# Kernel tuning notes

Measured on AMD Instinct MI355X. Metric: run time of the kernel, lower is better.

## Reference

```python
import jax, jax.numpy as jnp
import numpy as np

B, S, HID, NH, HD = 2, 2048, 1024, 16, 64
SCALE = 1.0 / np.sqrt(HD)
NEG = -1e9


def _rope_cache(seq_len, dim, base=10000.0):
    inv_freq = 1.0 / (base ** (np.arange(0, dim, 2, dtype=np.float32) / dim))
    t = np.arange(seq_len, dtype=np.float32)
    freqs = np.outer(t, inv_freq)                      # [S, dim/2]
    emb = np.concatenate([freqs, freqs], axis=-1)      # [S, dim]
    return jnp.asarray(np.cos(emb)), jnp.asarray(np.sin(emb))


def _rotate_half(x):
    x1, x2 = jnp.split(x, 2, axis=-1)
    return jnp.concatenate([-x2, x1], axis=-1)


def setup_inputs() -> dict:
    key = jax.random.key(0)
    k0, k1, k2, k3, k4 = jax.random.split(key, 5)
    hidden_states = jax.random.normal(k0, (B, S, HID), jnp.float32)
    Wq = jax.random.normal(k1, (HID, NH * HD), jnp.float32) * 0.02
    Wk = jax.random.normal(k2, (HID, NH * HD), jnp.float32) * 0.02
    Wv = jax.random.normal(k3, (HID, NH * HD), jnp.float32) * 0.02
    Wo = jax.random.normal(k4, (NH * HD, HID), jnp.float32) * 0.02
    causal = jnp.tril(jnp.ones((S, S), bool))
    attention_mask = jnp.broadcast_to(
        jnp.where(causal, 0.0, NEG).astype(jnp.float32)[None, None], (B, 1, S, S))
    position_ids = jnp.broadcast_to(jnp.arange(S, dtype=jnp.int32)[None], (B, S))
    cos, sin = _rope_cache(S, HD)
    return {"hidden_states": hidden_states, "attention_mask": attention_mask,
            "position_ids": position_ids, "cos": cos, "sin": sin,
            "Wq": Wq, "Wk": Wk, "Wv": Wv, "Wo": Wo}


def reference(hidden_states, attention_mask, position_ids, cos, sin, Wq, Wk, Wv, Wo):
    b, s, _ = hidden_states.shape
    def proj(W):  # [B,S,HID] @ [HID,NH*HD] -> [B,NH,S,HD]
        return jnp.einsum('bsh,hd->bsd', hidden_states, W).reshape(b, s, NH, HD).transpose(0, 2, 1, 3)
    q, k, v = proj(Wq), proj(Wk), proj(Wv)
    # RoPE: gather per-position cos/sin -> [B,1,S,HD]
    cos_g = cos[position_ids][:, None]
    sin_g = sin[position_ids][:, None]
    q = q * cos_g + _rotate_half(q) * sin_g
    k = k * cos_g + _rotate_half(k) * sin_g
    scores = jnp.einsum('bhqd,bhkd->bhqk', q, k) * SCALE + attention_mask
    attn = jax.nn.softmax(scores.astype(jnp.float32), axis=-1).astype(q.dtype)
    out = jnp.einsum('bhqk,bhkd->bhqd', attn, v)
    out = out.transpose(0, 2, 1, 3).reshape(b, s, NH * HD)
    return jnp.einsum('bsd,dh->bsh', out, Wo)
```

## Files before the change

kernel.cpp:

```cpp
#include <hip/hip_runtime.h>

typedef __bf16 bf16x8 __attribute__((ext_vector_type(8)));
typedef float  f32x4  __attribute__((ext_vector_type(4)));
typedef unsigned short ushortx8 __attribute__((ext_vector_type(8)));
typedef unsigned short ushortx4 __attribute__((ext_vector_type(4)));

static __device__ __forceinline__ unsigned short f2bf(float f) {
  unsigned int u = __builtin_bit_cast(unsigned int, f);
  u += 0x7FFFu + ((u >> 16) & 1u);
  return (unsigned short)(u >> 16);
}
static __device__ __forceinline__ unsigned short f2bf_fast(float f) {
  unsigned int u = __builtin_bit_cast(unsigned int, f);
  return (unsigned short)((u + 0x8000u) >> 16);
}

#define GLL16(gp, lp) __builtin_amdgcn_global_load_lds(                       \
    (const __attribute__((address_space(1))) void*)(gp),                      \
    (__attribute__((address_space(3))) void*)(lp), 16, 0, 0)

__global__ __launch_bounds__(256) void prep_kernel(const float* __restrict__ X,
                                                   const float* __restrict__ W0,
                                                   const float* __restrict__ W1,
                                                   const float* __restrict__ W2,
                                                   const float* __restrict__ W3,
                                                   unsigned short* __restrict__ Xbf,
                                                   unsigned short* __restrict__ D0,
                                                   unsigned short* __restrict__ D1,
                                                   unsigned short* __restrict__ D2,
                                                   unsigned short* __restrict__ D3) {
  int z = blockIdx.z;
  if (z >= 4) {
    long bid = (long)(z - 4) * 1024 + blockIdx.y * 32 + blockIdx.x;
    int tl = threadIdx.y * 32 + threadIdx.x;
    long i = bid * 2048 + (long)tl * 8;
    float4 f0 = *(const float4*)(X + i);
    float4 f1 = *(const float4*)(X + i + 4);
    ushortx8 u;
    u[0] = f2bf(f0.x); u[1] = f2bf(f0.y); u[2] = f2bf(f0.z); u[3] = f2bf(f0.w);
    u[4] = f2bf(f1.x); u[5] = f2bf(f1.y); u[6] = f2bf(f1.z); u[7] = f2bf(f1.w);
    *(ushortx8*)(Xbf + i) = u;
    return;
  }
  const float* src = (z == 0) ? W0 : (z == 1) ? W1 : (z == 2) ? W2 : W3;
  unsigned short* dst = (z == 0) ? D0 : (z == 1) ? D1 : (z == 2) ? D2 : D3;
  const int R = 1024, C = 1024;
  __shared__ unsigned short t[32][33];
  int c = blockIdx.x * 32 + threadIdx.x;
#pragma unroll
  for (int i = 0; i < 4; ++i) {
    int r = blockIdx.y * 32 + threadIdx.y + i * 8;
    t[threadIdx.y + i * 8][threadIdx.x] = f2bf(src[(size_t)r * C + c]);
  }
  __syncthreads();
  int rr = blockIdx.y * 32 + threadIdx.x;
#pragma unroll
  for (int i = 0; i < 4; ++i) {
    int cc = blockIdx.x * 32 + threadIdx.y + i * 8;
    dst[(size_t)cc * R + rr] = t[threadIdx.x][threadIdx.y + i * 8];
  }
}

__global__ __launch_bounds__(256, 3) void qkvr_kernel(
    const unsigned short* __restrict__ A,
    const unsigned short* __restrict__ BT0,
    const unsigned short* __restrict__ BT1,
    const unsigned short* __restrict__ BT2,
    unsigned short* __restrict__ outQ,
    unsigned short* __restrict__ outK,
    unsigned short* __restrict__ outVT,
    const int* __restrict__ pos_ids,
    const float* __restrict__ cosb,
    const float* __restrict__ sinb) {
  const int K = 1024;
  int id = blockIdx.x + 8 * (blockIdx.y + 32 * blockIdx.z);
  int m_idx = id & 31;
  int nzi = id >> 5;
  int n_idx = nzi & 7;
  int z = nzi >> 3;
  const unsigned short* BT = (z == 0) ? BT0 : (z == 1 ? BT1 : BT2);
  int n0 = n_idx * 128, m0 = m_idx * 128;
  int t = threadIdx.x, lane = t & 63, w = t >> 6;
  int wy = w >> 1, wx = w & 1;
  int n16 = lane & 15, quad = lane >> 4;

  __shared__ __align__(16) unsigned short sA[3][128][32];
  __shared__ __align__(16) unsigned short sB[3][128][32];
  __shared__ __align__(16) unsigned short sDummy[512];
  const int BUFE = 128 * 32;

  int r4 = lane >> 2, c4 = lane & 3;
  const char* gA = (const char*)(A + (size_t)(m0 + w * 32 + r4) * K) + ((c4 ^ (r4 & 3)) * 16);
  const char* gB = (const char*)(BT + (size_t)(n0 + w * 32 + r4) * K) + ((c4 ^ (r4 & 3)) * 16);
  const size_t row16 = (size_t)16 * K * 2;
  unsigned short* stA = &sA[0][w * 32][0];
  unsigned short* stB = &sB[0][w * 32][0];

  int cs = (quad ^ (n16 & 3)) * 8;
  const unsigned short* rdA = &sA[0][wy * 64 + n16][0] + cs;
  const unsigned short* rdB = &sB[0][wx * 64 + n16][0] + cs;

  f32x4 acc[4][4];
#pragma unroll
  for (int i = 0; i < 4; ++i)
#pragma unroll
    for (int j = 0; j < 4; ++j) acc[i][j] = f32x4{0.f, 0.f, 0.f, 0.f};

  bf16x8 a[4], b[4];

#define QSTG(tt, dA, dB)                                                        \
  do {                                                                          \
    GLL16(gA + (size_t)(tt) * 64, (dA));                                        \
    GLL16(gA + (size_t)(tt) * 64 + row16, (dA) + 16 * 32);                      \
    GLL16(gB + (size_t)(tt) * 64, (dB));                                        \
    GLL16(gB + (size_t)(tt) * 64 + row16, (dB) + 16 * 32);                      \
  } while (0)

#define QRD(bufi)                                                               \
  do {                                                                          \
    _Pragma("unroll") for (int i = 0; i < 4; ++i) {                             \
      a[i] = *(const bf16x8*)(rdA + (bufi) * BUFE + (i * 16) * 32);             \
      b[i] = *(const bf16x8*)(rdB + (bufi) * BUFE + (i * 16) * 32);             \
    }                                                                           \
  } while (0)

#define QMM                                                                     \
  do {                                                                          \
    _Pragma("unroll") for (int mt = 0; mt < 4; ++mt)                            \
      _Pragma("unroll") for (int nt = 0; nt < 4; ++nt)                          \
        acc[mt][nt] = __builtin_amdgcn_mfma_f32_16x16x32_bf16(                  \
            a[mt], b[nt], acc[mt][nt], 0, 0, 0);                                \
  } while (0)

  QSTG(0, stA, stB);
  QSTG(1, stA + BUFE, stB + BUFE);
  asm volatile("s_waitcnt vmcnt(4)" ::: "memory");
  __builtin_amdgcn_s_barrier();

#pragma unroll 3
  for (int kt = 0; kt < 30; ++kt) {
    int buf = kt % 3;
    int pfb = (kt + 2) % 3;
    QRD(buf);
    QSTG(kt + 2, stA + pfb * BUFE, stB + pfb * BUFE);
    QMM;
    asm volatile("s_waitcnt vmcnt(4)" ::: "memory");
    __builtin_amdgcn_s_barrier();
  }
  {
    QRD(0);
    QSTG(31, sDummy, sDummy);
    QMM;
    asm volatile("s_waitcnt vmcnt(4)" ::: "memory");
    __builtin_amdgcn_s_barrier();
  }
  {
    QRD(1);
    QSTG(31, sDummy, sDummy);
    QMM;
    asm volatile("s_waitcnt vmcnt(0)" ::: "memory");
  }
#undef QSTG
#undef QRD
#undef QMM

  if (z < 2) {
    const float qs = (z == 0) ? (0.125f * 1.44269504088896340736f) : 1.0f;
#pragma unroll
    for (int mt = 0; mt < 4; ++mt)
#pragma unroll
      for (int r = 0; r < 4; ++r) {
        int row = m0 + wy * 64 + mt * 16 + quad * 4 + r;
        int b_ = row >> 11, s_ = row & 2047;
        int pos = pos_ids[b_ * 2048 + s_];
        const float* cb = cosb + (size_t)pos * 64;
        const float* sb = sinb + (size_t)pos * 64;
#pragma unroll
        for (int nt = 0; nt < 2; ++nt) {
          int d0 = nt * 16 + n16;
          float c0 = cb[d0] * qs, s0 = sb[d0] * qs;
          float c1 = cb[d0 + 32] * qs, s1 = sb[d0 + 32] * qs;
          float x0 = acc[mt][nt][r], x1 = acc[mt][nt + 2][r];
          acc[mt][nt][r]     = x0 * c0 - x1 * s0;
          acc[mt][nt + 2][r] = x1 * c1 + x0 * s1;
        }
      }
    unsigned short* dst = (z == 0) ? outQ : outK;
#pragma unroll
    for (int mt = 0; mt < 4; ++mt)
#pragma unroll
      for (int nt = 0; nt < 4; ++nt)
#pragma unroll
        for (int r = 0; r < 4; ++r) {
          int row = m0 + wy * 64 + mt * 16 + quad * 4 + r;
          int col = n0 + wx * 64 + nt * 16 + n16;
          int b_ = row >> 11, s_ = row & 2047, h_ = col >> 6, d_ = col & 63;
          dst[(((size_t)b_ * 16 + h_) * 2048 + s_) * 64 + d_] = f2bf(acc[mt][nt][r]);
        }
    return;
  }

#pragma unroll
  for (int mt = 0; mt < 4; ++mt)
#pragma unroll
    for (int nt = 0; nt < 4; ++nt) {
      int row = m0 + wy * 64 + mt * 16 + quad * 4;
      int b_ = row >> 11, s_ = row & 2047;
      int col = n0 + wx * 64 + nt * 16 + n16;
      int h_ = col >> 6, d_ = col & 63;
      ushortx4 u;
#pragma unroll
      for (int r = 0; r < 4; ++r) u[r] = f2bf(acc[mt][nt][r]);
      *(ushortx4*)(&outVT[(((size_t)b_ * 16 + h_) * 64 + d_) * 2048 + s_]) = u;
    }
}

__global__ __launch_bounds__(256) void wor_kernel(const unsigned short* __restrict__ A,
                                                  const unsigned short* __restrict__ BT,
                                                  float* __restrict__ outF) {
  const int K = 1024, N = 1024;
  int id = blockIdx.x + 8 * blockIdx.y;
  int m_idx = id & 31, n_idx = id >> 5;
  int m0 = m_idx * 128, n0 = n_idx * 64;
  int t = threadIdx.x, lane = t & 63, w = t >> 6;
  int wy = w >> 1, wx = w & 1;
  int n16 = lane & 15, quad = lane >> 4;

  __shared__ __align__(16) unsigned short sA[3][128][32];
  __shared__ __align__(16) unsigned short sB[3][64][32];
  __shared__ __align__(16) unsigned short sDummy[512];
  const int BUFA = 128 * 32, BUFB = 64 * 32;

  int r4 = lane >> 2, c4 = lane & 3;
  const char* gA = (const char*)(A + (size_t)(m0 + w * 32 + r4) * K) + ((c4 ^ (r4 & 3)) * 16);
  const char* gB = (const char*)(BT + (size_t)(n0 + w * 16 + r4) * K) + ((c4 ^ (r4 & 3)) * 16);
  const size_t row16 = (size_t)16 * K * 2;
  unsigned short* stA = &sA[0][w * 32][0];
  unsigned short* stB = &sB[0][w * 16][0];

  int cs = (quad ^ (n16 & 3)) * 8;
  const unsigned short* rdA = &sA[0][wy * 64 + n16][0] + cs;
  const unsigned short* rdB = &sB[0][wx * 32 + n16][0] + cs;

  f32x4 acc[4][2];
#pragma unroll
  for (int i = 0; i < 4; ++i)
#pragma unroll
    for (int j = 0; j < 2; ++j) acc[i][j] = f32x4{0.f, 0.f, 0.f, 0.f};

  bf16x8 a[4], b[2];

#define WSTG(tt, dA, dB)                                                        \
  do {                                                                          \
    GLL16(gA + (size_t)(tt) * 64, (dA));                                        \
    GLL16(gA + (size_t)(tt) * 64 + row16, (dA) + 16 * 32);                      \
    GLL16(gB + (size_t)(tt) * 64, (dB));                                        \
  } while (0)

#define WRD(bufi)                                                               \
  do {                                                                          \
    _Pragma("unroll") for (int i = 0; i < 4; ++i)                               \
      a[i] = *(const bf16x8*)(rdA + (bufi) * BUFA + (i * 16) * 32);             \
    _Pragma("unroll") for (int j = 0; j < 2; ++j)                               \
      b[j] = *(const bf16x8*)(rdB + (bufi) * BUFB + (j * 16) * 32);             \
  } while (0)

#define WMM                                                                     \
  do {                                                                          \
    _Pragma("unroll") for (int mt = 0; mt < 4; ++mt)                            \
      _Pragma("unroll") for (int nt = 0; nt < 2; ++nt)                          \
        acc[mt][nt] = __builtin_amdgcn_mfma_f32_16x16x32_bf16(                  \
            a[mt], b[nt], acc[mt][nt], 0, 0, 0);                                \
  } while (0)

  WSTG(0, stA, stB);
  WSTG(1, stA + BUFA, stB + BUFB);
  asm volatile("s_waitcnt vmcnt(3)" ::: "memory");
  __builtin_amdgcn_s_barrier();

#pragma unroll 3
  for (int kt = 0; kt < 30; ++kt) {
    int buf = kt % 3;
    int pfb = (kt + 2) % 3;
    WRD(buf);
    WSTG(kt + 2, stA + pfb * BUFA, stB + pfb * BUFB);
    WMM;
    asm volatile("s_waitcnt vmcnt(3)" ::: "memory");
    __builtin_amdgcn_s_barrier();
  }
  {
    WRD(0);
    WSTG(31, sDummy, sDummy);
    WMM;
    asm volatile("s_waitcnt vmcnt(3)" ::: "memory");
    __builtin_amdgcn_s_barrier();
  }
  {
    WRD(1);
    WSTG(31, sDummy, sDummy);
    WMM;
    asm volatile("s_waitcnt vmcnt(0)" ::: "memory");
  }
#undef WSTG
#undef WRD
#undef WMM

#pragma unroll
  for (int mt = 0; mt < 4; ++mt)
#pragma unroll
    for (int nt = 0; nt < 2; ++nt)
#pragma unroll
      for (int r = 0; r < 4; ++r) {
        int row = m0 + wy * 64 + mt * 16 + quad * 4 + r;
        int col = n0 + wx * 32 + nt * 16 + n16;
        outF[(size_t)row * N + col] = acc[mt][nt][r];
      }
}

__global__ __launch_bounds__(512) void attn_kernel(const unsigned short* __restrict__ Q,
                                                   const unsigned short* __restrict__ Kk,
                                                   const unsigned short* __restrict__ VT,
                                                   unsigned short* __restrict__ O) {
  int bh = blockIdx.x;
  int qt = (int)(gridDim.y - 1 - blockIdx.y);
  int t = threadIdx.x;
  int lane = t & 63;
  int w = t >> 6;
  int g = w >> 2;
  int w4 = w & 3;
  int n16 = lane & 15, quad = lane >> 4;
  int r8 = lane >> 3, c8 = lane & 7;
  const unsigned short* Qb = Q + (size_t)bh * 2048 * 64;
  const unsigned short* Kb = Kk + (size_t)bh * 2048 * 64;
  const unsigned short* Vb = VT + (size_t)bh * 64 * 2048;

  __shared__ __align__(16) unsigned short sKV[2 * 2 * 2 * 4096];
  __shared__ __align__(16) unsigned short sP[8][16 * 64];
  unsigned short* spW = sP[w];
  unsigned short* gBase = sKV + g * 16384;

  int b_ = bh >> 4, h_ = bh & 15;
  int nk = qt + 1;
  int u = (nk + 1) >> 1;
  int beg = g ? u : 0;
  int end = g ? nk : u;
  int qg = qt * 64 + w4 * 16 + n16;

  bf16x8 aQ[2];
#pragma unroll
  for (int kb = 0; kb < 2; ++kb)
    aQ[kb] = *(const bf16x8*)(Qb + (size_t)qg * 64 + kb * 32 + quad * 8);

  f32x4 o[4];
  float mst = -3e38f, lst = 0.f;
#pragma unroll
  for (int ct = 0; ct < 4; ++ct) o[ct] = f32x4{0.f, 0.f, 0.f, 0.f};

#define ASTAGE(kt_, BUF)                                                                  \
  do {                                                                                    \
    const unsigned short* kg_ = Kb + (size_t)((kt_) * 64 + w4 * 16) * 64;                 \
    const unsigned short* vg_ = Vb + (size_t)(w4 * 16) * 2048 + (kt_) * 64;               \
    unsigned short* dK = gBase + (BUF) * 8192 + (w4 * 16) * 64;                           \
    unsigned short* dV = dK + 4096;                                                       \
    GLL16(kg_ + (size_t)r8 * 64 + (c8 ^ r8) * 8, dK);                                     \
    GLL16(kg_ + (size_t)(8 + r8) * 64 + (c8 ^ r8) * 8, dK + 8 * 64);                      \
    GLL16(vg_ + (size_t)r8 * 2048 + (c8 ^ r8) * 8, dV);                                   \
    GLL16(vg_ + (size_t)(8 + r8) * 2048 + (c8 ^ r8) * 8, dV + 8 * 64);                    \
  } while (0)

#define ACOMPUTE(kt_, BUF)                                                                \
  do {                                                                                    \
    const unsigned short* kT_ = gBase + (BUF) * 8192;                                     \
    const unsigned short* vT_ = kT_ + 4096;                                               \
    f32x4 sc[4];                                \
    _Pragma("unroll") for (int mt = 0; mt < 4; ++mt) {                                    \
      const unsigned short* kr = &kT_[(mt * 16 + n16) * 64];                              \
      bf16x8 ka0 = *(const bf16x8*)(kr + ((quad ^ (n16 & 7)) * 8));                       \
      bf16x8 ka1 = *(const bf16x8*)(kr + (((4 + quad) ^ (n16 & 7)) * 8));                 \
      f32x4 zv = f32x4{0.f, 0.f, 0.f, 0.f};                                               \
      zv = __builtin_amdgcn_mfma_f32_16x16x32_bf16(ka0, aQ[0], zv, 0, 0, 0);              \
      sc[mt] = __builtin_amdgcn_mfma_f32_16x16x32_bf16(ka1, aQ[1], zv, 0, 0, 0);          \
    }                                                                                     \
    float p[4][4];                                                                        \
    _Pragma("unroll") for (int mt = 0; mt < 4; ++mt)                                      \
      _Pragma("unroll") for (int r = 0; r < 4; ++r) p[mt][r] = sc[mt][r];                 \
    if ((kt_) == nk - 1) {                                 \
      int kb0 = (kt_) * 64 + quad * 4;                                                    \
      _Pragma("unroll") for (int mt = 0; mt < 4; ++mt)                                    \
        _Pragma("unroll") for (int r = 0; r < 4; ++r)                                     \
          if (kb0 + mt * 16 + r > qg) p[mt][r] = -3e38f;                                  \
    }                                                                                     \
    float rm = p[0][0];                                                                   \
    _Pragma("unroll") for (int mt = 0; mt < 4; ++mt)                                      \
      _Pragma("unroll") for (int r = 0; r < 4; ++r) rm = fmaxf(rm, p[mt][r]);             \
    rm = fmaxf(rm, __shfl_xor(rm, 16));                                                   \
    rm = fmaxf(rm, __shfl_xor(rm, 32));                                                   \
    if (!__all(rm <= mst + 8.f)) {        \
      float mn = fmaxf(mst, rm);                                                          \
      float al = exp2f(mst - mn);                                                         \
      mst = mn;                                                                           \
      lst *= al;                                                                          \
      _Pragma("unroll") for (int ct = 0; ct < 4; ++ct)                                    \
        _Pragma("unroll") for (int r = 0; r < 4; ++r) o[ct][r] *= al;                     \
    }                                                                                     \
    float rs = 0.f;                                                                       \
    _Pragma("unroll") for (int mt = 0; mt < 4; ++mt)                                      \
      _Pragma("unroll") for (int r = 0; r < 4; ++r) {                                     \
        p[mt][r] = exp2f(p[mt][r] - mst);                                                 \
        rs += p[mt][r];                                                                   \
      }                                                                                   \
    lst += rs;                                                                            \
    _Pragma("unroll") for (int mt = 0; mt < 4; ++mt) {                                    \
      ushortx4 uu;                                                                        \
      _Pragma("unroll") for (int r = 0; r < 4; ++r) uu[r] = f2bf_fast(p[mt][r]);          \
      int ch = (mt * 2 + (quad >> 1)) ^ (n16 & 7);                                        \
      *(ushortx4*)(&spW[n16 * 64 + ch * 8 + (quad & 1) * 4]) = uu;                        \
    }                                                                                     \
    __builtin_amdgcn_s_waitcnt(0xC07F);     \
    bf16x8 aP0 = *(const bf16x8*)(&spW[n16 * 64 + ((quad ^ (n16 & 7)) * 8)]);             \
    bf16x8 aP1 = *(const bf16x8*)(&spW[n16 * 64 + (((4 + quad) ^ (n16 & 7)) * 8)]);       \
    _Pragma("unroll") for (int ct = 0; ct < 4; ++ct) {                                    \
      const unsigned short* vr = &vT_[(ct * 16 + n16) * 64];                              \
      bf16x8 va0 = *(const bf16x8*)(vr + ((quad ^ (n16 & 7)) * 8));                       \
      bf16x8 va1 = *(const bf16x8*)(vr + (((4 + quad) ^ (n16 & 7)) * 8));                 \
      o[ct] = __builtin_amdgcn_mfma_f32_16x16x32_bf16(va0, aP0, o[ct], 0, 0, 0);          \
      o[ct] = __builtin_amdgcn_mfma_f32_16x16x32_bf16(va1, aP1, o[ct], 0, 0, 0);          \
    }                                                                                     \
  } while (0)

  if (beg < end) ASTAGE(beg, 0);
  int it = 0;
  while (it < u) {
    __syncthreads();
    {
      int kt = beg + it;
      if (kt + 1 < end) ASTAGE(kt + 1, 1);
      if (kt < end) ACOMPUTE(kt, 0);
    }
    if (++it >= u) break;
    __syncthreads();
    {
      int kt = beg + it;
      if (kt + 1 < end) ASTAGE(kt + 1, 0);
      if (kt < end) ACOMPUTE(kt, 1);
    }
    ++it;
  }
#undef ASTAGE
#undef ACOMPUTE

  lst += __shfl_xor(lst, 16);
  lst += __shfl_xor(lst, 32);

  __syncthreads();
  float* scratch = (float*)sKV;
  int sidx = (w4 * 64 + lane) * 18;
  if (g == 1) {
#pragma unroll
    for (int ct = 0; ct < 4; ++ct)
#pragma unroll
      for (int r = 0; r < 4; ++r) scratch[sidx + ct * 4 + r] = o[ct][r];
    scratch[sidx + 16] = mst;
    scratch[sidx + 17] = lst;
  }
  __syncthreads();
  if (g == 0) {
    float m1 = scratch[sidx + 16], l1 = scratch[sidx + 17];
    float m = fmaxf(mst, m1);
    float a0 = exp2f(mst - m), a1 = exp2f(m1 - m);
    float inv = 1.0f / (lst * a0 + l1 * a1);
#pragma unroll
    for (int ct = 0; ct < 4; ++ct) {
      ushortx4 uo;
#pragma unroll
      for (int r = 0; r < 4; ++r) {
        float v = (o[ct][r] * a0 + scratch[sidx + ct * 4 + r] * a1) * inv;
        uo[r] = f2bf(v);
      }
      size_t addr = ((size_t)b_ * 2048 + qg) * 1024 + h_ * 64 + ct * 16 + quad * 4;
      *(ushortx4*)(&O[addr]) = uo;
    }
  }
}

extern "C" void kernel_launch(void* const* d_in, const int* in_sizes, int n_in,
                              void* d_out, int out_size, void* d_ws, size_t ws_size,
                              hipStream_t stream) {
  const float* X    = (const float*)d_in[0];
  const int*   pos  = (const int*)d_in[2];
  const float* cosb = (const float*)d_in[3];
  const float* sinb = (const float*)d_in[4];
  const float* Wq   = (const float*)d_in[5];
  const float* Wk   = (const float*)d_in[6];
  const float* Wv   = (const float*)d_in[7];
  const float* Wo   = (const float*)d_in[8];
  float* out = (float*)d_out;

  char* ws = (char*)d_ws;
  const size_t SZ_X = 4096UL * 1024 * 2;
  const size_t SZ_W = 1024UL * 1024 * 2;
  unsigned short* Xbf = (unsigned short*)(ws);
  unsigned short* WTq = (unsigned short*)(ws + SZ_X);
  unsigned short* WTk = (unsigned short*)(ws + SZ_X + SZ_W);
  unsigned short* WTv = (unsigned short*)(ws + SZ_X + 2 * SZ_W);
  unsigned short* WTo = (unsigned short*)(ws + SZ_X + 3 * SZ_W);
  unsigned short* Qbf = (unsigned short*)(ws + SZ_X + 4 * SZ_W);
  unsigned short* Kbf = (unsigned short*)(ws + 2 * SZ_X + 4 * SZ_W);
  unsigned short* VTr = (unsigned short*)(ws + 3 * SZ_X + 4 * SZ_W);
  unsigned short* Obf = (unsigned short*)(ws + 4 * SZ_X + 4 * SZ_W);

  prep_kernel<<<dim3(32, 32, 6), dim3(32, 8), 0, stream>>>(
      X, Wq, Wk, Wv, Wo, Xbf, WTq, WTk, WTv, WTo);

  qkvr_kernel<<<dim3(8, 32, 3), 256, 0, stream>>>(Xbf, WTq, WTk, WTv,
                                                  Qbf, Kbf, VTr,
                                                  pos, cosb, sinb);

  attn_kernel<<<dim3(32, 32), 512, 0, stream>>>(Qbf, Kbf, VTr, Obf);

  wor_kernel<<<dim3(8, 64), 256, 0, stream>>>(Obf, WTo, out);
}
```

Baseline: 201.7 us.

## Drop split-KV across two warp groups in causal attention kernel

The attention kernel previously split each query tile's key range between two groups of four waves and merged their partial softmax states through shared memory. The change removes the split, so one group of four waves walks the whole causal key range with double buffering, and the cross-group merge is gone. This halves threads and shared memory per block, allowing more resident blocks and removing the merge and two barriers. The cost is a longer serial loop per block, which may lengthen the critical path for the long diagonal tiles.

```diff
diff --git a/kernel.cpp b/kernel.cpp
--- a/kernel.cpp
+++ b/kernel.cpp
@@ -317,7 +317,7 @@
       }
 }
 
-__global__ __launch_bounds__(512) void attn_kernel(const unsigned short* __restrict__ Q,
+__global__ __launch_bounds__(256) void attn_kernel(const unsigned short* __restrict__ Q,
                                                    const unsigned short* __restrict__ Kk,
                                                    const unsigned short* __restrict__ VT,
                                                    unsigned short* __restrict__ O) {
@@ -326,25 +326,19 @@
   int t = threadIdx.x;
   int lane = t & 63;
   int w = t >> 6;
-  int g = w >> 2;
-  int w4 = w & 3;
   int n16 = lane & 15, quad = lane >> 4;
   int r8 = lane >> 3, c8 = lane & 7;
   const unsigned short* Qb = Q + (size_t)bh * 2048 * 64;
   const unsigned short* Kb = Kk + (size_t)bh * 2048 * 64;
   const unsigned short* Vb = VT + (size_t)bh * 64 * 2048;
 
-  __shared__ __align__(16) unsigned short sKV[2 * 2 * 2 * 4096];
-  __shared__ __align__(16) unsigned short sP[8][16 * 64];
+  __shared__ __align__(16) unsigned short sKV[2 * 8192];
+  __shared__ __align__(16) unsigned short sP[4][16 * 64];
   unsigned short* spW = sP[w];
-  unsigned short* gBase = sKV + g * 16384;
 
   int b_ = bh >> 4, h_ = bh & 15;
   int nk = qt + 1;
-  int u = (nk + 1) >> 1;
-  int beg = g ? u : 0;
-  int end = g ? nk : u;
-  int qg = qt * 64 + w4 * 16 + n16;
+  int qg = qt * 64 + w * 16 + n16;
 
   bf16x8 aQ[2];
 #pragma unroll
@@ -358,9 +352,9 @@
 
 #define ASTAGE(kt_, BUF)                                                                  \
   do {                                                                                    \
-    const unsigned short* kg_ = Kb + (size_t)((kt_) * 64 + w4 * 16) * 64;                 \
-    const unsigned short* vg_ = Vb + (size_t)(w4 * 16) * 2048 + (kt_) * 64;               \
-    unsigned short* dK = gBase + (BUF) * 8192 + (w4 * 16) * 64;                           \
+    const unsigned short* kg_ = Kb + (size_t)((kt_) * 64 + w * 16) * 64;                  \
+    const unsigned short* vg_ = Vb + (size_t)(w * 16) * 2048 + (kt_) * 64;                \
+    unsigned short* dK = sKV + (BUF) * 8192 + (w * 16) * 64;                              \
     unsigned short* dV = dK + 4096;                                                       \
     GLL16(kg_ + (size_t)r8 * 64 + (c8 ^ r8) * 8, dK);                                     \
     GLL16(kg_ + (size_t)(8 + r8) * 64 + (c8 ^ r8) * 8, dK + 8 * 64);                      \
@@ -370,7 +364,7 @@
 
 #define ACOMPUTE(kt_, BUF)                                                                \
   do {                                                                                    \
-    const unsigned short* kT_ = gBase + (BUF) * 8192;                                     \
+    const unsigned short* kT_ = sKV + (BUF) * 8192;                                       \
     const unsigned short* vT_ = kT_ + 4096;                                               \
     f32x4 sc[4];                                \
     _Pragma("unroll") for (int mt = 0; mt < 4; ++mt) {                                    \
@@ -428,21 +422,21 @@
     }                                                                                     \
   } while (0)
 
-  if (beg < end) ASTAGE(beg, 0);
+  ASTAGE(0, 0);
   int it = 0;
-  while (it < u) {
+  while (it < nk) {
     __syncthreads();
     {
-      int kt = beg + it;
-      if (kt + 1 < end) ASTAGE(kt + 1, 1);
-      if (kt < end) ACOMPUTE(kt, 0);
+      int kt = it;
+      if (kt + 1 < nk) ASTAGE(kt + 1, 1);
+      ACOMPUTE(kt, 0);
     }
-    if (++it >= u) break;
+    if (++it >= nk) break;
     __syncthreads();
     {
-      int kt = beg + it;
-      if (kt + 1 < end) ASTAGE(kt + 1, 0);
-      if (kt < end) ACOMPUTE(kt, 1);
+      int kt = it;
+      if (kt + 1 < nk) ASTAGE(kt + 1, 0);
+      ACOMPUTE(kt, 1);
     }
     ++it;
   }
@@ -451,35 +445,14 @@
 
   lst += __shfl_xor(lst, 16);
   lst += __shfl_xor(lst, 32);
-
-  __syncthreads();
-  float* scratch = (float*)sKV;
-  int sidx = (w4 * 64 + lane) * 18;
-  if (g == 1) {
-#pragma unroll
-    for (int ct = 0; ct < 4; ++ct)
-#pragma unroll
-      for (int r = 0; r < 4; ++r) scratch[sidx + ct * 4 + r] = o[ct][r];
-    scratch[sidx + 16] = mst;
-    scratch[sidx + 17] = lst;
-  }
-  __syncthreads();
-  if (g == 0) {
-    float m1 = scratch[sidx + 16], l1 = scratch[sidx + 17];
-    float m = fmaxf(mst, m1);
-    float a0 = exp2f(mst - m), a1 = exp2f(m1 - m);
-    float inv = 1.0f / (lst * a0 + l1 * a1);
-#pragma unroll
-    for (int ct = 0; ct < 4; ++ct) {
-      ushortx4 uo;
-#pragma unroll
-      for (int r = 0; r < 4; ++r) {
-        float v = (o[ct][r] * a0 + scratch[sidx + ct * 4 + r] * a1) * inv;
-        uo[r] = f2bf(v);
-      }
-      size_t addr = ((size_t)b_ * 2048 + qg) * 1024 + h_ * 64 + ct * 16 + quad * 4;
-      *(ushortx4*)(&O[addr]) = uo;
-    }
+  float inv = 1.0f / lst;
+#pragma unroll
+  for (int ct = 0; ct < 4; ++ct) {
+    ushortx4 uo;
+#pragma unroll
+    for (int r = 0; r < 4; ++r) uo[r] = f2bf(o[ct][r] * inv);
+    size_t addr = ((size_t)b_ * 2048 + qg) * 1024 + h_ * 64 + ct * 16 + quad * 4;
+    *(ushortx4*)(&O[addr]) = uo;
   }
 }
 
@@ -516,7 +489,7 @@
                                                   Qbf, Kbf, VTr,
                                                   pos, cosb, sinb);
 
-  attn_kernel<<<dim3(32, 32), 512, 0, stream>>>(Qbf, Kbf, VTr, Obf);
+  attn_kernel<<<dim3(32, 32), 256, 0, stream>>>(Qbf, Kbf, VTr, Obf);
 
   wor_kernel<<<dim3(8, 64), 256, 0, stream>>>(Obf, WTo, out);
 }
```

Result: no change. 201.6 us (-0.1%).
